# Kernel tuning notes

Measured on AMD Instinct MI355X. Metric: run time of the kernel, lower is better.

The kernel has to match this reference:

```python
import jax, jax.numpy as jnp
import numpy as np

N_NODES = 50000
N_RAND_EDGES = 800000
D = 128


def setup_inputs() -> dict:
    key = jax.random.key(0)
    ks = jax.random.split(key, 16)
    # random edges + self loops (docstring: self loops added to avoid zero in-degree)
    src_r = jax.random.randint(ks[0], (N_RAND_EDGES,), 0, N_NODES, dtype=jnp.int32)
    dst_r = jax.random.randint(ks[1], (N_RAND_EDGES,), 0, N_NODES, dtype=jnp.int32)
    loop = jnp.arange(N_NODES, dtype=jnp.int32)
    src = jnp.concatenate([src_r, loop])
    dst = jnp.concatenate([dst_r, loop])
    E = src.shape[0]
    edge_weight = jax.random.uniform(ks[2], (E,), dtype=jnp.float32, minval=0.05, maxval=1.0)
    feats = jax.random.normal(ks[3], (N_NODES, D), dtype=jnp.float32)
    s = 1.0 / np.sqrt(D)
    params = {}
    for i in range(3):
        params[f'W_self{i}'] = jax.random.normal(ks[4 + 3 * i], (D, D), dtype=jnp.float32) * s
        params[f'W_neigh{i}'] = jax.random.normal(ks[5 + 3 * i], (D, D), dtype=jnp.float32) * s
        params[f'b{i}'] = jnp.zeros((D,), dtype=jnp.float32)
    return dict(feats=feats, edge_weight=edge_weight,
                W_self0=params['W_self0'], W_neigh0=params['W_neigh0'], b0=params['b0'],
                W_self1=params['W_self1'], W_neigh1=params['W_neigh1'], b1=params['b1'],
                W_self2=params['W_self2'], W_neigh2=params['W_neigh2'], b2=params['b2'],
                src=src, dst=dst)


def reference(feats, edge_weight, W_self0, W_neigh0, b0, W_self1, W_neigh1, b1,
              W_self2, W_neigh2, b2, src, dst):
    N = feats.shape[0]
    seg = lambda x, ids: jax.ops.segment_sum(x, ids, num_segments=N)
    # EdgeWeightNorm('both'): w_ij / sqrt(out_deg_w(src) * in_deg_w(dst))
    deg_dst = seg(edge_weight, dst)  # weighted in-degree [N]
    deg_src = seg(edge_weight, src)  # weighted out-degree [N]
    denom = jnp.sqrt(jnp.maximum(deg_src[src] * deg_dst[dst], 1e-12))
    w = edge_weight / denom  # [E]
    # unweighted in-degree for DGL fn.mean
    in_deg = jnp.maximum(seg(jnp.ones_like(edge_weight), dst), 1.0)  # [N]

    def sage_layer(h, Ws, Wn, b, act):
        # GraphNorm(None) is identity. SAGEConv mean aggregator with edge weights:
        # m_e = w_e * h[src_e]; neigh_v = mean over in-edges of v
        msgs = w[:, None] * h[src]            # [E, D] (memory-bound gather)
        neigh = seg(msgs, dst) / in_deg[:, None]  # [N, D]
        out = h @ Ws + neigh @ Wn + b
        return jax.nn.relu(out) if act else out

    h = sage_layer(feats, W_self0, W_neigh0, b0, True)
    h = sage_layer(h, W_self1, W_neigh1, b1, True)
    h = sage_layer(h, W_self2, W_neigh2, b2, False)
    return h
```

## Files before the change

### kernel.cpp

```cpp
#include <hip/hip_runtime.h>
#include <hip/hip_bf16.h>

#define D 128
#define BS 256
#define CHUNK 4096

typedef __attribute__((ext_vector_type(8))) short short8v;
typedef __attribute__((ext_vector_type(4))) float f32x4;

__device__ __forceinline__ ushort f2bf(float f) {
    uint u = __float_as_uint(f);
    return (ushort)((u + 0x7fffu + ((u >> 16) & 1u)) >> 16);
}
__device__ __forceinline__ float bf2f(ushort s) {
    return __uint_as_float(((uint)s) << 16);
}


__global__ void hist_kernel(const int* __restrict__ src, const int* __restrict__ dst,
                            int* __restrict__ H, int E, int EB, int NB) {
    __shared__ int hD[256], hS[256];
    int tid = threadIdx.x, blk = blockIdx.x;
    hD[tid] = 0; hS[tid] = 0;
    __syncthreads();
    int e0 = blk * CHUNK;
    int e1 = e0 + CHUNK < E ? e0 + CHUNK : E;
    for (int e = e0 + tid; e < e1; e += BS) {
        atomicAdd(&hD[dst[e] >> 8], 1);
        atomicAdd(&hS[src[e] >> 8], 1);
    }
    __syncthreads();
    if (tid < NB) {
        H[tid * EB + blk] = hD[tid];
        H[NB * EB + tid * EB + blk] = hS[tid];
    }
}

__global__ void scanA(const int* __restrict__ H, int* __restrict__ tmp,
                      int* __restrict__ bsum, int L) {
    __shared__ int s[512];
    int tid = threadIdx.x;
    int i = blockIdx.x * 512 + tid;
    int v = (i < L) ? H[i] : 0;
    s[tid] = v;
    __syncthreads();
    for (int off = 1; off < 512; off <<= 1) {
        int t = (tid >= off) ? s[tid - off] : 0;
        __syncthreads();
        s[tid] += t;
        __syncthreads();
    }
    if (i < L) tmp[i] = s[tid];
    if (tid == 511) bsum[blockIdx.x] = s[511];
}

__global__ void scanB(const int* __restrict__ bsum, int* __restrict__ boff, int nb) {
    __shared__ int s[512];
    int tid = threadIdx.x;
    int v = (tid < nb) ? bsum[tid] : 0;
    s[tid] = v;
    __syncthreads();
    for (int off = 1; off < 512; off <<= 1) {
        int t = (tid >= off) ? s[tid - off] : 0;
        __syncthreads();
        s[tid] += t;
        __syncthreads();
    }
    if (tid < nb) boff[tid] = s[tid] - v;
}

__global__ void scanC(int* __restrict__ H, const int* __restrict__ tmp,
                      const int* __restrict__ boff, int L) {
    int i = blockIdx.x * 512 + threadIdx.x;
    if (i < L) H[i] = tmp[i] + boff[blockIdx.x] - H[i];
}

__global__ void partition_kernel(const int* __restrict__ src, const int* __restrict__ dst,
                                 const float* __restrict__ ew, const int* __restrict__ H,
                                 int2* __restrict__ bufD, int2* __restrict__ bufS,
                                 int E, int EB, int NB) {
    __shared__ int curD[256], curS[256];
    int tid = threadIdx.x, blk = blockIdx.x;
    if (tid < NB) {
        curD[tid] = H[tid * EB + blk];
        curS[tid] = H[NB * EB + tid * EB + blk] - E;
    }
    __syncthreads();
    int e0 = blk * CHUNK;
    int e1 = e0 + CHUNK < E ? e0 + CHUNK : E;
    for (int e = e0 + tid; e < e1; e += BS) {
        int s = src[e], d = dst[e];
        int w = __float_as_int(ew[e]);
        int pD = atomicAdd(&curD[d >> 8], 1);
        bufD[pD] = make_int2(((d & 255) << 16) | s, w);
        int pS = atomicAdd(&curS[s >> 8], 1);
        bufS[pS] = make_int2(s, w);
    }
}

__global__ void srcdeg_kernel(const int2* __restrict__ bufS, const int* __restrict__ H,
                              float* __restrict__ rs, int E, int EB, int NB, int N) {
    __shared__ float acc[256];
    int tid = threadIdx.x, b = blockIdx.x;
    acc[tid] = 0.f;
    __syncthreads();
    int base = H[NB * EB + b * EB] - E;
    int end = (b + 1 < NB) ? H[NB * EB + (b + 1) * EB] - E : E;
    for (int i = base + tid; i < end; i += BS) {
        int2 v = bufS[i];
        atomicAdd(&acc[v.x & 255], __int_as_float(v.y));
    }
    __syncthreads();
    int node = (b << 8) + tid;
    if (node < N) rs[node] = rsqrtf(acc[tid]);
}

__global__ void csr_kernel(const int2* __restrict__ bufD, const int* __restrict__ H,
                           const float* __restrict__ rs, int* __restrict__ rowp,
                           int2* __restrict__ csr, int E, int EB, int NB, int N) {
    __shared__ int lcnt[256];
    __shared__ float lw[256];
    __shared__ int sc[256];
    int tid = threadIdx.x, b = blockIdx.x;
    lcnt[tid] = 0; lw[tid] = 0.f;
    __syncthreads();
    int base = H[b * EB];
    int end = (b + 1 < NB) ? H[(b + 1) * EB] : E;
    for (int i = base + tid; i < end; i += BS) {
        int2 v = bufD[i];
        int l = v.x >> 16;
        atomicAdd(&lcnt[l], 1);
        atomicAdd(&lw[l], __int_as_float(v.y));
    }
    __syncthreads();
    int myc = lcnt[tid];
    float myw = lw[tid];
    sc[tid] = myc;
    __syncthreads();
    for (int off = 1; off < 256; off <<= 1) {
        int t = (tid >= off) ? sc[tid - off] : 0;
        __syncthreads();
        sc[tid] += t;
        __syncthreads();
    }
    int lbase = base + sc[tid] - myc;
    int node = (b << 8) + tid;
    if (node < N) rowp[node] = lbase;
    if (b == 0 && tid == 0) rowp[N] = E;
    lcnt[tid] = lbase;
    lw[tid] = (myc > 0) ? rsqrtf(myw) / (float)myc : 0.f;
    __syncthreads();
    for (int i = base + tid; i < end; i += BS) {
        int2 v = bufD[i];
        int l = v.x >> 16;
        int s = v.x & 0xFFFF;
        float w = __int_as_float(v.y) * rs[s] * lw[l];
        int p = atomicAdd(&lcnt[l], 1);
        csr[p] = make_int2(s, __float_as_int(w));
    }
}


__global__ void cvt_feats(const float* __restrict__ f, ushort* __restrict__ hb, int n8) {
    int i = blockIdx.x * 256 + threadIdx.x;
    if (i >= n8) return;
    const float4* f4 = (const float4*)f + (size_t)i * 2;
    float4 a = f4[0], b = f4[1];
    uint4 o;
    o.x = (uint)f2bf(a.x) | ((uint)f2bf(a.y) << 16);
    o.y = (uint)f2bf(a.z) | ((uint)f2bf(a.w) << 16);
    o.z = (uint)f2bf(b.x) | ((uint)f2bf(b.y) << 16);
    o.w = (uint)f2bf(b.z) | ((uint)f2bf(b.w) << 16);
    *((uint4*)hb + i) = o;
}

__global__ void cvt_w(const float* __restrict__ Ws, const float* __restrict__ Wn,
                      ushort* __restrict__ Wt) {
    int n = blockIdx.x;
    int k = threadIdx.x;
    float v = (k < 128) ? Ws[k * D + n] : Wn[(k - 128) * D + n];
    Wt[n * 256 + k] = f2bf(v);
}


__global__ void aggregate_bf(const ushort* __restrict__ h, const int* __restrict__ rowp,
                             const int2* __restrict__ csr, ushort* __restrict__ nb, int N) {
    int node = (blockIdx.x * blockDim.x + threadIdx.x) >> 6;
    int lane = threadIdx.x & 63;
    if (node >= N) return;
    int beg = rowp[node], end = rowp[node + 1];
    float ax0 = 0.f, ay0 = 0.f, ax1 = 0.f, ay1 = 0.f;
    float ax2 = 0.f, ay2 = 0.f, ax3 = 0.f, ay3 = 0.f;
    int i = beg;
    for (; i + 4 <= end; i += 4) {
        int2 e0 = csr[i], e1 = csr[i + 1], e2 = csr[i + 2], e3 = csr[i + 3];
        float w0 = __int_as_float(e0.y), w1 = __int_as_float(e1.y);
        float w2 = __int_as_float(e2.y), w3 = __int_as_float(e3.y);
        uint x0 = *(const uint*)(h + (size_t)e0.x * D + 2 * lane);
        uint x1 = *(const uint*)(h + (size_t)e1.x * D + 2 * lane);
        uint x2 = *(const uint*)(h + (size_t)e2.x * D + 2 * lane);
        uint x3 = *(const uint*)(h + (size_t)e3.x * D + 2 * lane);
        ax0 += w0 * bf2f((ushort)x0); ay0 += w0 * bf2f((ushort)(x0 >> 16));
        ax1 += w1 * bf2f((ushort)x1); ay1 += w1 * bf2f((ushort)(x1 >> 16));
        ax2 += w2 * bf2f((ushort)x2); ay2 += w2 * bf2f((ushort)(x2 >> 16));
        ax3 += w3 * bf2f((ushort)x3); ay3 += w3 * bf2f((ushort)(x3 >> 16));
    }
    for (; i < end; ++i) {
        int2 e0 = csr[i];
        float w0 = __int_as_float(e0.y);
        uint x0 = *(const uint*)(h + (size_t)e0.x * D + 2 * lane);
        ax0 += w0 * bf2f((ushort)x0); ay0 += w0 * bf2f((ushort)(x0 >> 16));
    }
    float rx = (ax0 + ax1) + (ax2 + ax3);
    float ry = (ay0 + ay1) + (ay2 + ay3);
    uint o = (uint)f2bf(rx) | ((uint)f2bf(ry) << 16);
    *(uint*)(nb + (size_t)node * D + 2 * lane) = o;
}


#define AST2 40

__global__ __launch_bounds__(256) void mfma_gemm(
    const ushort* __restrict__ A1, const ushort* __restrict__ A2,
    const ushort* __restrict__ Wt, const float* __restrict__ bias,
    ushort* __restrict__ outb, float* __restrict__ outf, int N, int relu) {
    __shared__ ushort As[2][128][AST2];
    __shared__ ushort Bs[2][128][AST2];

    int tid = threadIdx.x;
    int lane = tid & 63;
    int w = tid >> 6;
    int m0 = (w >> 1) * 64, n0 = (w & 1) * 64;
    int row0 = blockIdx.x * 128;
    int q = lane >> 4, li = lane & 15;

    int r1 = tid >> 2, c = tid & 3;
    int gr1 = min(row0 + r1, N - 1);
    int gr2 = min(row0 + r1 + 64, N - 1);

    uint4 sa0, sa1, sb0, sb1;

    sa0 = *(const uint4*)(A1 + (size_t)gr1 * D + c * 8);
    sa1 = *(const uint4*)(A1 + (size_t)gr2 * D + c * 8);
    sb0 = *(const uint4*)(Wt + (size_t)r1 * 256 + c * 8);
    sb1 = *(const uint4*)(Wt + (size_t)(r1 + 64) * 256 + c * 8);
    *(uint4*)&As[0][r1][c * 8] = sa0;
    *(uint4*)&As[0][r1 + 64][c * 8] = sa1;
    *(uint4*)&Bs[0][r1][c * 8] = sb0;
    *(uint4*)&Bs[0][r1 + 64][c * 8] = sb1;
    __syncthreads();

    f32x4 zero = {0.f, 0.f, 0.f, 0.f};
    f32x4 acc[4][4];
    #pragma unroll
    for (int mf = 0; mf < 4; ++mf)
        #pragma unroll
        for (int nf = 0; nf < 4; ++nf) acc[mf][nf] = zero;

    for (int kc = 0; kc < 8; ++kc) {
        int b = kc & 1;
        if (kc < 7) {
            int nc = kc + 1;
            const ushort* Ak = ((nc < 4) ? A1 : A2) + (nc & 3) * 32;
            sa0 = *(const uint4*)(Ak + (size_t)gr1 * D + c * 8);
            sa1 = *(const uint4*)(Ak + (size_t)gr2 * D + c * 8);
            const ushort* Wk = Wt + nc * 32;
            sb0 = *(const uint4*)(Wk + (size_t)r1 * 256 + c * 8);
            sb1 = *(const uint4*)(Wk + (size_t)(r1 + 64) * 256 + c * 8);
        }

        union FragU { uint2 u[2]; short8v v; };
        FragU fa[4], fb[4];
        #pragma unroll
        for (int mf = 0; mf < 4; ++mf) {
            const ushort* p = &As[b][m0 + mf * 16 + li][0];
            fa[mf].u[0] = *(const uint2*)(p + 4 * q);
            fa[mf].u[1] = *(const uint2*)(p + 16 + 4 * q);
        }
        #pragma unroll
        for (int nf = 0; nf < 4; ++nf) {
            const ushort* p = &Bs[b][n0 + nf * 16 + li][0];
            fb[nf].u[0] = *(const uint2*)(p + 4 * q);
            fb[nf].u[1] = *(const uint2*)(p + 16 + 4 * q);
        }
        #pragma unroll
        for (int mf = 0; mf < 4; ++mf)
            #pragma unroll
            for (int nf = 0; nf < 4; ++nf)
                acc[mf][nf] = __builtin_amdgcn_mfma_f32_16x16x32_bf16(
                    fa[mf].v, fb[nf].v, acc[mf][nf], 0, 0, 0);

        if (kc < 7) {
            int b2 = b ^ 1;
            *(uint4*)&As[b2][r1][c * 8] = sa0;
            *(uint4*)&As[b2][r1 + 64][c * 8] = sa1;
            *(uint4*)&Bs[b2][r1][c * 8] = sb0;
            *(uint4*)&Bs[b2][r1 + 64][c * 8] = sb1;
        }
        __syncthreads();
    }

    #pragma unroll
    for (int nf = 0; nf < 4; ++nf) {
        int n = n0 + nf * 16 + li;
        float bn = bias[n];
        #pragma unroll
        for (int mf = 0; mf < 4; ++mf) {
            #pragma unroll
            for (int p = 0; p < 4; ++p) {
                int gr = row0 + m0 + mf * 16 + q * 4 + p;
                if (gr >= N) continue;
                float v = acc[mf][nf][p] + bn;
                if (relu) v = fmaxf(v, 0.f);
                if (outf) outf[(size_t)gr * D + n] = v;
                else outb[(size_t)gr * D + n] = f2bf(v);
            }
        }
    }
}


extern "C" void kernel_launch(void* const* d_in, const int* in_sizes, int n_in,
                              void* d_out, int out_size, void* d_ws, size_t ws_size,
                              hipStream_t stream) {
    const float* feats = (const float*)d_in[0];
    const float* ew    = (const float*)d_in[1];
    const float* Wself[3]  = {(const float*)d_in[2], (const float*)d_in[5], (const float*)d_in[8]};
    const float* Wneigh[3] = {(const float*)d_in[3], (const float*)d_in[6], (const float*)d_in[9]};
    const float* bias[3]   = {(const float*)d_in[4], (const float*)d_in[7], (const float*)d_in[10]};
    const int* src = (const int*)d_in[11];
    const int* dst = (const int*)d_in[12];

    int N = in_sizes[0] / D;
    int E = in_sizes[11];
    int NB = (N + 255) >> 8;
    int EB = (E + CHUNK - 1) / CHUNK;
    int L = 2 * NB * EB;
    int sblocks = (L + 511) / 512;

    char* ws = (char*)d_ws;
    size_t p = 0;
    auto align256 = [&]() { p = (p + 255) & ~(size_t)255; };

    int* H    = (int*)(ws + p); p += (size_t)L * 4;        align256();
    int* tmp  = (int*)(ws + p); p += (size_t)L * 4;        align256();
    int* bsum = (int*)(ws + p); p += 512 * 4;              align256();
    int* boff = (int*)(ws + p); p += 512 * 4;              align256();
    int2* bufD = (int2*)(ws + p); p += (size_t)E * 8;      align256();
    int2* bufS = (int2*)(ws + p); p += (size_t)E * 8;      align256();
    int2* csr  = bufS;
    int* rowp  = (int*)(ws + p);   p += (size_t)(N + 1) * 4; align256();
    float* rs  = (float*)(ws + p); p += (size_t)N * 4;       align256();
    ushort* hA = (ushort*)(ws + p); p += (size_t)N * D * 2;  align256();
    ushort* hB = (ushort*)(ws + p); p += (size_t)N * D * 2;  align256();
    ushort* nb = (ushort*)(ws + p); p += (size_t)N * D * 2;  align256();
    ushort* Wt = (ushort*)(ws + p); p += (size_t)3 * 128 * 256 * 2; align256();
    (void)ws_size; (void)n_in; (void)out_size;

    hist_kernel<<<EB, BS, 0, stream>>>(src, dst, H, E, EB, NB);
    scanA<<<sblocks, 512, 0, stream>>>(H, tmp, bsum, L);
    scanB<<<1, 512, 0, stream>>>(bsum, boff, sblocks);
    scanC<<<sblocks, 512, 0, stream>>>(H, tmp, boff, L);
    partition_kernel<<<EB, BS, 0, stream>>>(src, dst, ew, H, bufD, bufS, E, EB, NB);
    srcdeg_kernel<<<NB, BS, 0, stream>>>(bufS, H, rs, E, EB, NB, N);
    csr_kernel<<<NB, BS, 0, stream>>>(bufD, H, rs, rowp, csr, E, EB, NB, N);

    int n8 = N * D / 8;
    cvt_feats<<<(n8 + 255) / 256, 256, 0, stream>>>(feats, hA, n8);
    for (int Lr = 0; Lr < 3; ++Lr)
        cvt_w<<<128, 256, 0, stream>>>(Wself[Lr], Wneigh[Lr], Wt + (size_t)Lr * 32768);

    int gb = (N + 127) / 128;
    ushort* hin = hA;
    ushort* houts[3] = {hB, hA, nullptr};
    for (int Lr = 0; Lr < 3; ++Lr) {
        aggregate_bf<<<(N + 3) / 4, 256, 0, stream>>>(hin, rowp, csr, nb, N);
        mfma_gemm<<<gb, 256, 0, stream>>>(hin, nb, Wt + (size_t)Lr * 32768, bias[Lr],
                                          houts[Lr], (Lr == 2) ? (float*)d_out : nullptr,
                                          N, (Lr < 2) ? 1 : 0);
        hin = houts[Lr];
    }
}
```

Measured before the change: 245.2 us.

## Replace histogram+scan CSR build with fixed-capacity buckets and fuse conversions

Result: faster. 231.9 us (-5.4%).

```diff
diff --git a/kernel.cpp b/kernel.cpp
--- a/kernel.cpp
+++ b/kernel.cpp
@@ -4,6 +4,7 @@
 #define D 128
 #define BS 256
 #define CHUNK 4096
+#define CAP 8192
 
 typedef __attribute__((ext_vector_type(8))) short short8v;
 typedef __attribute__((ext_vector_type(4))) float f32x4;
@@ -17,9 +18,48 @@
 }
 
 
-__global__ void hist_kernel(const int* __restrict__ src, const int* __restrict__ dst,
-                            int* __restrict__ H, int E, int EB, int NB) {
+__global__ void cvt_all(const float* __restrict__ feats,
+                        const float* __restrict__ Ws0, const float* __restrict__ Wn0,
+                        const float* __restrict__ Ws1, const float* __restrict__ Wn1,
+                        const float* __restrict__ Ws2, const float* __restrict__ Wn2,
+                        ushort* __restrict__ hb, ushort* __restrict__ Wt,
+                        int* __restrict__ cursD, int* __restrict__ cursS,
+                        int n8, int FB) {
+    int tid = threadIdx.x;
+    if (blockIdx.x == 0) {
+        cursD[tid] = tid * CAP;
+        cursS[tid] = tid * CAP;
+    }
+    if (blockIdx.x < FB) {
+        int i = blockIdx.x * 256 + tid;
+        if (i >= n8) return;
+        const float4* f4 = (const float4*)feats + (size_t)i * 2;
+        float4 a = f4[0], b = f4[1];
+        uint4 o;
+        o.x = (uint)f2bf(a.x) | ((uint)f2bf(a.y) << 16);
+        o.y = (uint)f2bf(a.z) | ((uint)f2bf(a.w) << 16);
+        o.z = (uint)f2bf(b.x) | ((uint)f2bf(b.y) << 16);
+        o.w = (uint)f2bf(b.z) | ((uint)f2bf(b.w) << 16);
+        *((uint4*)hb + i) = o;
+        return;
+    }
+    int wb = blockIdx.x - FB;
+    int layer = wb >> 7;
+    int n = wb & 127;
+    int k = tid;
+    const float* Ws = (layer == 0) ? Ws0 : (layer == 1) ? Ws1 : Ws2;
+    const float* Wn = (layer == 0) ? Wn0 : (layer == 1) ? Wn1 : Wn2;
+    float v = (k < 128) ? Ws[k * D + n] : Wn[(k - 128) * D + n];
+    Wt[(size_t)layer * 32768 + n * 256 + k] = f2bf(v);
+}
+
+
+__global__ void partition_kernel(const int* __restrict__ src, const int* __restrict__ dst,
+                                 const float* __restrict__ ew,
+                                 int* __restrict__ cursD, int* __restrict__ cursS,
+                                 int2* __restrict__ bufD, int2* __restrict__ bufS, int E) {
     __shared__ int hD[256], hS[256];
+    __shared__ int bD[256], bS[256];
     int tid = threadIdx.x, blk = blockIdx.x;
     hD[tid] = 0; hS[tid] = 0;
     __syncthreads();
@@ -30,82 +70,29 @@
         atomicAdd(&hS[src[e] >> 8], 1);
     }
     __syncthreads();
-    if (tid < NB) {
-        H[tid * EB + blk] = hD[tid];
-        H[NB * EB + tid * EB + blk] = hS[tid];
-    }
-}
-
-__global__ void scanA(const int* __restrict__ H, int* __restrict__ tmp,
-                      int* __restrict__ bsum, int L) {
-    __shared__ int s[512];
-    int tid = threadIdx.x;
-    int i = blockIdx.x * 512 + tid;
-    int v = (i < L) ? H[i] : 0;
-    s[tid] = v;
-    __syncthreads();
-    for (int off = 1; off < 512; off <<= 1) {
-        int t = (tid >= off) ? s[tid - off] : 0;
-        __syncthreads();
-        s[tid] += t;
-        __syncthreads();
-    }
-    if (i < L) tmp[i] = s[tid];
-    if (tid == 511) bsum[blockIdx.x] = s[511];
-}
-
-__global__ void scanB(const int* __restrict__ bsum, int* __restrict__ boff, int nb) {
-    __shared__ int s[512];
-    int tid = threadIdx.x;
-    int v = (tid < nb) ? bsum[tid] : 0;
-    s[tid] = v;
-    __syncthreads();
-    for (int off = 1; off < 512; off <<= 1) {
-        int t = (tid >= off) ? s[tid - off] : 0;
-        __syncthreads();
-        s[tid] += t;
-        __syncthreads();
-    }
-    if (tid < nb) boff[tid] = s[tid] - v;
-}
-
-__global__ void scanC(int* __restrict__ H, const int* __restrict__ tmp,
-                      const int* __restrict__ boff, int L) {
-    int i = blockIdx.x * 512 + threadIdx.x;
-    if (i < L) H[i] = tmp[i] + boff[blockIdx.x] - H[i];
-}
-
-__global__ void partition_kernel(const int* __restrict__ src, const int* __restrict__ dst,
-                                 const float* __restrict__ ew, const int* __restrict__ H,
-                                 int2* __restrict__ bufD, int2* __restrict__ bufS,
-                                 int E, int EB, int NB) {
-    __shared__ int curD[256], curS[256];
-    int tid = threadIdx.x, blk = blockIdx.x;
-    if (tid < NB) {
-        curD[tid] = H[tid * EB + blk];
-        curS[tid] = H[NB * EB + tid * EB + blk] - E;
-    }
-    __syncthreads();
-    int e0 = blk * CHUNK;
-    int e1 = e0 + CHUNK < E ? e0 + CHUNK : E;
+    int cD = hD[tid], cS = hS[tid];
+    if (cD > 0) bD[tid] = atomicAdd(&cursD[tid], cD);
+    if (cS > 0) bS[tid] = atomicAdd(&cursS[tid], cS);
+    __syncthreads();
     for (int e = e0 + tid; e < e1; e += BS) {
         int s = src[e], d = dst[e];
         int w = __float_as_int(ew[e]);
-        int pD = atomicAdd(&curD[d >> 8], 1);
+        int pD = atomicAdd(&bD[d >> 8], 1);
         bufD[pD] = make_int2(((d & 255) << 16) | s, w);
-        int pS = atomicAdd(&curS[s >> 8], 1);
+        int pS = atomicAdd(&bS[s >> 8], 1);
         bufS[pS] = make_int2(s, w);
     }
 }
 
-__global__ void srcdeg_kernel(const int2* __restrict__ bufS, const int* __restrict__ H,
-                              float* __restrict__ rs, int E, int EB, int NB, int N) {
+
+__global__ void srcdeg_kernel(const int2* __restrict__ bufS, const int* __restrict__ cursS,
+                              float* __restrict__ rs, int N) {
     __shared__ float acc[256];
     int tid = threadIdx.x, b = blockIdx.x;
     acc[tid] = 0.f;
     __syncthreads();
-    int base = H[NB * EB + b * EB] - E;
-    int end = (b + 1 < NB) ? H[NB * EB + (b + 1) * EB] - E : E;
+    int base = b * CAP;
+    int end = cursS[b];
     for (int i = base + tid; i < end; i += BS) {
         int2 v = bufS[i];
         atomicAdd(&acc[v.x & 255], __int_as_float(v.y));
@@ -115,17 +102,18 @@
     if (node < N) rs[node] = rsqrtf(acc[tid]);
 }
 
-__global__ void csr_kernel(const int2* __restrict__ bufD, const int* __restrict__ H,
-                           const float* __restrict__ rs, int* __restrict__ rowp,
-                           int2* __restrict__ csr, int E, int EB, int NB, int N) {
+
+__global__ void csr_kernel(const int2* __restrict__ bufD, const int* __restrict__ cursD,
+                           const float* __restrict__ rs, int2* __restrict__ begend,
+                           int2* __restrict__ csrb, int N) {
     __shared__ int lcnt[256];
     __shared__ float lw[256];
     __shared__ int sc[256];
     int tid = threadIdx.x, b = blockIdx.x;
     lcnt[tid] = 0; lw[tid] = 0.f;
     __syncthreads();
-    int base = H[b * EB];
-    int end = (b + 1 < NB) ? H[(b + 1) * EB] : E;
+    int base = b * CAP;
+    int end = cursD[b];
     for (int i = base + tid; i < end; i += BS) {
         int2 v = bufD[i];
         int l = v.x >> 16;
@@ -145,8 +133,7 @@
     }
     int lbase = base + sc[tid] - myc;
     int node = (b << 8) + tid;
-    if (node < N) rowp[node] = lbase;
-    if (b == 0 && tid == 0) rowp[N] = E;
+    if (node < N) begend[node] = make_int2(lbase, base + sc[tid]);
     lcnt[tid] = lbase;
     lw[tid] = (myc > 0) ? rsqrtf(myw) / (float)myc : 0.f;
     __syncthreads();
@@ -156,39 +143,18 @@
         int s = v.x & 0xFFFF;
         float w = __int_as_float(v.y) * rs[s] * lw[l];
         int p = atomicAdd(&lcnt[l], 1);
-        csr[p] = make_int2(s, __float_as_int(w));
-    }
-}
-
-
-__global__ void cvt_feats(const float* __restrict__ f, ushort* __restrict__ hb, int n8) {
-    int i = blockIdx.x * 256 + threadIdx.x;
-    if (i >= n8) return;
-    const float4* f4 = (const float4*)f + (size_t)i * 2;
-    float4 a = f4[0], b = f4[1];
-    uint4 o;
-    o.x = (uint)f2bf(a.x) | ((uint)f2bf(a.y) << 16);
-    o.y = (uint)f2bf(a.z) | ((uint)f2bf(a.w) << 16);
-    o.z = (uint)f2bf(b.x) | ((uint)f2bf(b.y) << 16);
-    o.w = (uint)f2bf(b.z) | ((uint)f2bf(b.w) << 16);
-    *((uint4*)hb + i) = o;
-}
-
-__global__ void cvt_w(const float* __restrict__ Ws, const float* __restrict__ Wn,
-                      ushort* __restrict__ Wt) {
-    int n = blockIdx.x;
-    int k = threadIdx.x;
-    float v = (k < 128) ? Ws[k * D + n] : Wn[(k - 128) * D + n];
-    Wt[n * 256 + k] = f2bf(v);
-}
-
-
-__global__ void aggregate_bf(const ushort* __restrict__ h, const int* __restrict__ rowp,
+        csrb[p] = make_int2(s, __float_as_int(w));
+    }
+}
+
+
+__global__ void aggregate_bf(const ushort* __restrict__ h, const int2* __restrict__ begend,
                              const int2* __restrict__ csr, ushort* __restrict__ nb, int N) {
     int node = (blockIdx.x * blockDim.x + threadIdx.x) >> 6;
     int lane = threadIdx.x & 63;
     if (node >= N) return;
-    int beg = rowp[node], end = rowp[node + 1];
+    int2 be = begend[node];
+    int beg = be.x, end = be.y;
     float ax0 = 0.f, ay0 = 0.f, ax1 = 0.f, ay1 = 0.f;
     float ax2 = 0.f, ay2 = 0.f, ax3 = 0.f, ay3 = 0.f;
     int i = beg;
@@ -335,46 +301,37 @@
     int E = in_sizes[11];
     int NB = (N + 255) >> 8;
     int EB = (E + CHUNK - 1) / CHUNK;
-    int L = 2 * NB * EB;
-    int sblocks = (L + 511) / 512;
 
     char* ws = (char*)d_ws;
     size_t p = 0;
     auto align256 = [&]() { p = (p + 255) & ~(size_t)255; };
 
-    int* H    = (int*)(ws + p); p += (size_t)L * 4;        align256();
-    int* tmp  = (int*)(ws + p); p += (size_t)L * 4;        align256();
-    int* bsum = (int*)(ws + p); p += 512 * 4;              align256();
-    int* boff = (int*)(ws + p); p += 512 * 4;              align256();
-    int2* bufD = (int2*)(ws + p); p += (size_t)E * 8;      align256();
-    int2* bufS = (int2*)(ws + p); p += (size_t)E * 8;      align256();
-    int2* csr  = bufS;
-    int* rowp  = (int*)(ws + p);   p += (size_t)(N + 1) * 4; align256();
-    float* rs  = (float*)(ws + p); p += (size_t)N * 4;       align256();
-    ushort* hA = (ushort*)(ws + p); p += (size_t)N * D * 2;  align256();
-    ushort* hB = (ushort*)(ws + p); p += (size_t)N * D * 2;  align256();
-    ushort* nb = (ushort*)(ws + p); p += (size_t)N * D * 2;  align256();
+    int* cursD = (int*)(ws + p); p += 256 * 4;             align256();
+    int* cursS = (int*)(ws + p); p += 256 * 4;             align256();
+    int2* bufD = (int2*)(ws + p); p += (size_t)NB * CAP * 8; align256();
+    int2* bufS = (int2*)(ws + p); p += (size_t)NB * CAP * 8; align256();
+    int2* csrb = (int2*)(ws + p); p += (size_t)NB * CAP * 8; align256();
+    int2* begend = (int2*)(ws + p); p += (size_t)N * 8;    align256();
+    float* rs  = (float*)(ws + p); p += (size_t)N * 4;     align256();
+    ushort* hA = (ushort*)(ws + p); p += (size_t)N * D * 2; align256();
+    ushort* hB = (ushort*)(ws + p); p += (size_t)N * D * 2; align256();
+    ushort* nb = (ushort*)(ws + p); p += (size_t)N * D * 2; align256();
     ushort* Wt = (ushort*)(ws + p); p += (size_t)3 * 128 * 256 * 2; align256();
     (void)ws_size; (void)n_in; (void)out_size;
 
-    hist_kernel<<<EB, BS, 0, stream>>>(src, dst, H, E, EB, NB);
-    scanA<<<sblocks, 512, 0, stream>>>(H, tmp, bsum, L);
-    scanB<<<1, 512, 0, stream>>>(bsum, boff, sblocks);
-    scanC<<<sblocks, 512, 0, stream>>>(H, tmp, boff, L);
-    partition_kernel<<<EB, BS, 0, stream>>>(src, dst, ew, H, bufD, bufS, E, EB, NB);
-    srcdeg_kernel<<<NB, BS, 0, stream>>>(bufS, H, rs, E, EB, NB, N);
-    csr_kernel<<<NB, BS, 0, stream>>>(bufD, H, rs, rowp, csr, E, EB, NB, N);
-
     int n8 = N * D / 8;
-    cvt_feats<<<(n8 + 255) / 256, 256, 0, stream>>>(feats, hA, n8);
-    for (int Lr = 0; Lr < 3; ++Lr)
-        cvt_w<<<128, 256, 0, stream>>>(Wself[Lr], Wneigh[Lr], Wt + (size_t)Lr * 32768);
+    int FB = (n8 + 255) / 256;
+    cvt_all<<<FB + 384, 256, 0, stream>>>(feats, Wself[0], Wneigh[0], Wself[1], Wneigh[1],
+                                          Wself[2], Wneigh[2], hA, Wt, cursD, cursS, n8, FB);
+    partition_kernel<<<EB, BS, 0, stream>>>(src, dst, ew, cursD, cursS, bufD, bufS, E);
+    srcdeg_kernel<<<NB, BS, 0, stream>>>(bufS, cursS, rs, N);
+    csr_kernel<<<NB, BS, 0, stream>>>(bufD, cursD, rs, begend, csrb, N);
 
     int gb = (N + 127) / 128;
     ushort* hin = hA;
     ushort* houts[3] = {hB, hA, nullptr};
     for (int Lr = 0; Lr < 3; ++Lr) {
-        aggregate_bf<<<(N + 3) / 4, 256, 0, stream>>>(hin, rowp, csr, nb, N);
+        aggregate_bf<<<(N + 3) / 4, 256, 0, stream>>>(hin, begend, csrb, nb, N);
         mfma_gemm<<<gb, 256, 0, stream>>>(hin, nb, Wt + (size_t)Lr * 32768, bias[Lr],
                                           houts[Lr], (Lr == 2) ? (float*)d_out : nullptr,
                                           N, (Lr < 2) ? 1 : 0);
```
